# Kernel optimization log

Measured on AMD Instinct MI355X. Metric: run time of the kernel, lower is better.

The kernel has to match this reference:

```python
import jax, jax.numpy as jnp
import numpy as np

N = 25000      # nodes
E = 400000     # directed edges (avg degree 16)
FN = 32        # node feature dim
FE = 16        # edge feature dim
H = 16         # hidden_state_size
M = 16         # message_size
ITERS = 3      # mp_iterations


def setup_inputs() -> dict:
    key = jax.random.key(0)
    ks = jax.random.split(key, 16)
    s = 0.1
    return {
        "node_features": jax.random.normal(ks[0], (N, FN), jnp.float32),
        "edge_features": jax.random.normal(ks[1], (E, FE), jnp.float32),
        # Initial dense
        "W_init": jax.random.normal(ks[2], (FN, H), jnp.float32) * s,
        "b_init": jnp.zeros((H,), jnp.float32),
        # edge_net dense: FE -> M*H
        "W_edge": jax.random.normal(ks[3], (FE, M * H), jnp.float32) * s,
        "b_edge": jnp.zeros((M * H,), jnp.float32),
        # GRU (keras default, reset_after=True), input dim 1, units H, gate order z|r|h
        "Wi_gru": jax.random.normal(ks[4], (1, 3 * H), jnp.float32) * s,
        "Wh_gru": jax.random.normal(ks[5], (H, 3 * H), jnp.float32) * s,
        "bi_gru": jnp.zeros((3 * H,), jnp.float32),
        "bh_gru": jnp.zeros((3 * H,), jnp.float32),
        # Readout denses -> 1 output
        "W_ri": jax.random.normal(ks[6], (2 * H, 1), jnp.float32) * s,
        "b_ri": jnp.zeros((1,), jnp.float32),
        "W_rj": jax.random.normal(ks[7], (H, 1), jnp.float32) * s,
        "b_rj": jnp.zeros((1,), jnp.float32),
        # graph structure (directed edges): message to `receivers[e]` from `senders[e]`
        "receivers": jax.random.randint(ks[8], (E,), 0, N, jnp.int32),
        "senders": jax.random.randint(ks[9], (E,), 0, N, jnp.int32),
    }


def _gru_seq(seq, Wi, Wh, bi, bh):
    # seq: [N, T] sequence of scalars per node; keras GRU, reset_after=True, units=H
    n = seq.shape[0]
    xs = seq.T[:, :, None]  # [T, N, 1]
    h0 = jnp.zeros((n, H), seq.dtype)

    def step(h, x_t):
        gx = x_t @ Wi + bi            # [N, 3H]
        gh = h @ Wh + bh              # [N, 3H]
        xz, xr, xh = jnp.split(gx, 3, axis=1)
        hz, hr, hh = jnp.split(gh, 3, axis=1)
        z = jax.nn.sigmoid(xz + hz)
        r = jax.nn.sigmoid(xr + hr)
        hcand = jnp.tanh(xh + r * hh)
        h_new = z * h + (1.0 - z) * hcand
        return h_new, None

    h_final, _ = jax.lax.scan(step, h0, xs)
    return h_final


def reference(node_features, edge_features, W_init, b_init, W_edge, b_edge,
              Wi_gru, Wh_gru, bi_gru, bh_gru, W_ri, b_ri, W_rj, b_rj,
              receivers, senders):
    # Initial hidden state
    hidden0 = node_features @ W_init + b_init   # [N, H]
    hidden = hidden0

    # edge_net(edge) reshaped to per-edge matrices [E, M, H] (constant across iterations)
    edge_mats = (edge_features @ W_edge + b_edge).reshape(E, M, H)

    for _ in range(ITERS):
        h_nb = hidden[senders]                                  # [E, H]
        msg = jnp.einsum("emh,eh->em", edge_mats, h_nb)        # [E, M] matvec per edge
        messages = jax.ops.segment_sum(msg, receivers, num_segments=N)  # sum aggregation
        seq = jnp.concatenate([hidden, messages], axis=1)       # [N, H+M]
        hidden = _gru_seq(seq, Wi_gru, Wh_gru, bi_gru, bh_gru)  # [N, H]

    # Readout
    i = jnp.concatenate([hidden, hidden0], axis=1) @ W_ri + b_ri  # [N, 1]
    j = hidden @ W_rj + b_rj                                      # [N, 1]
    return jnp.sum(i * j, axis=0)                                 # [1]
```

## Files before the change

kernel.cpp:

```cpp
#include <hip/hip_runtime.h>

#define N_NODES 25000
#define N_EDGES 400000

__device__ __forceinline__ float fast_sigmoid(float x) {
    return __builtin_amdgcn_rcpf(1.0f + __expf(-x));
}
__device__ __forceinline__ float fast_tanh(float x) {
    return 1.0f - 2.0f * __builtin_amdgcn_rcpf(__expf(2.0f * x) + 1.0f);
}

#define SWZF(x, k) __int_as_float(__builtin_amdgcn_ds_swizzle(__float_as_int(x), ((k) << 10) | 0x1F))
#define BCAST16(x, t) __int_as_float(__builtin_amdgcn_ds_swizzle(__float_as_int(x), ((t) << 5) | 0x10))

__global__ void __launch_bounds__(256) k_init(
        const float* __restrict__ nf, const float* __restrict__ Wini,
        const float* __restrict__ bini,
        float* __restrict__ hidden0, float* __restrict__ hid,
        int* __restrict__ cnt, int* __restrict__ rcnt)
{
    int gtid = blockIdx.x * 256 + threadIdx.x;
    if (gtid <= N_NODES) { cnt[gtid] = 0; rcnt[gtid] = 0; }
    int node = gtid >> 4;
    int j = gtid & 15;
    if (node >= N_NODES) return;

    const float4* nf4 = (const float4*)(nf + node * 32);
    float acc = bini[j];
#pragma unroll
    for (int g = 0; g < 8; ++g) {
        float4 v = nf4[g];
        acc = fmaf(v.x, Wini[(g*4+0)*16 + j], acc);
        acc = fmaf(v.y, Wini[(g*4+1)*16 + j], acc);
        acc = fmaf(v.z, Wini[(g*4+2)*16 + j], acc);
        acc = fmaf(v.w, Wini[(g*4+3)*16 + j], acc);
    }
    hidden0[node*16 + j] = acc;
    hid[node*16 + j] = acc;
}

__global__ void __launch_bounds__(256) k_rank(const int* __restrict__ send,
        const int* __restrict__ recv,
        int* __restrict__ cnt, int* __restrict__ rcnt,
        int* __restrict__ rank_s, int* __restrict__ rank_r)
{
    int e = blockIdx.x * 256 + threadIdx.x;
    if (e < N_EDGES) {
        rank_s[e] = atomicAdd(&cnt[send[e]], 1);
        rank_r[e] = atomicAdd(&rcnt[recv[e]], 1);
    }
}

#define SCAN_TOT 25600
__global__ void __launch_bounds__(1024) k_scan2(
        const int* __restrict__ cnt,  int* __restrict__ row_ptr,
        const int* __restrict__ rcnt, int* __restrict__ rrow_ptr,
        float* __restrict__ out)
{
    __shared__ int data[SCAN_TOT];
    __shared__ int sums[1024];
    int t = threadIdx.x;
    const int CH = 25;

    const int* SRC = blockIdx.x ? rcnt : cnt;
    int* DST = blockIdx.x ? rrow_ptr : row_ptr;

    for (int i = t; i < SCAN_TOT; i += 1024)
        data[i] = (i < N_NODES) ? SRC[i] : 0;
    __syncthreads();

    int base = t * CH;
    int s = 0;
#pragma unroll
    for (int i = 0; i < CH; ++i) s += data[base + i];
    sums[t] = s;
    __syncthreads();

    for (int off = 1; off < 1024; off <<= 1) {
        int add = (t >= off) ? sums[t - off] : 0;
        __syncthreads();
        sums[t] += add;
        __syncthreads();
    }
    int run = sums[t] - s;

#pragma unroll
    for (int i = 0; i < CH; ++i) {
        int v = data[base + i];
        data[base + i] = run;
        run += v;
    }
    __syncthreads();

    for (int i = t; i < N_NODES; i += 1024)
        DST[i] = data[i];
    if (t == 0) {
        if (blockIdx.x == 0) { row_ptr[N_NODES] = N_EDGES; out[0] = 0.0f; }
        else                 { rrow_ptr[N_NODES] = N_EDGES; }
    }
}

__global__ void __launch_bounds__(256) k_place(const int* __restrict__ send,
        const int* __restrict__ recv,
        const int* __restrict__ rank_s, const int* __restrict__ rank_r,
        const int* __restrict__ row_ptr, const int* __restrict__ rrow_ptr,
        const float* __restrict__ ef, float* __restrict__ efp,
        int* __restrict__ rp)
{
    int e = blockIdx.x * 256 + threadIdx.x;
    if (e < N_EDGES) {
        int pos = row_ptr[send[e]] + rank_s[e];
        rp[pos] = rrow_ptr[recv[e]] + rank_r[e];
        const float4* src = (const float4*)(ef + (size_t)e * 16);
        float4* dst = (float4*)(efp + (size_t)pos * 16);
        float4 a = src[0], b = src[1], c = src[2], d = src[3];
        dst[0] = a; dst[1] = b; dst[2] = c; dst[3] = d;
    }
}

#define MCHUNK 512
#define MSG16(E0,E1,E2,E3) ( \
    ( fmaf((E0).w,q[3],  fmaf((E0).z,q[2],  fmaf((E0).y,q[1],  fmaf((E0).x,q[0],  qb)))) \
    + fmaf((E1).w,q[7],  fmaf((E1).z,q[6],  fmaf((E1).y,q[5],  fmaf((E1).x,q[4],  0.0f)))) ) \
  + ( fmaf((E2).w,q[11], fmaf((E2).z,q[10], fmaf((E2).y,q[9],  fmaf((E2).x,q[8],  0.0f)))) \
    + fmaf((E3).w,q[15], fmaf((E3).z,q[14], fmaf((E3).y,q[13], fmaf((E3).x,q[12], 0.0f)))) ) )

__global__ void __launch_bounds__(256) k_msg(
        const float* __restrict__ hid, const float* __restrict__ efp,
        const int* __restrict__ rp,
        const float* __restrict__ We, const float* __restrict__ be,
        const int* __restrict__ row_ptr,
        float* __restrict__ tmp)
{
    __shared__ float sef[MCHUNK * 16];
    __shared__ int   srp[MCHUNK];
    int tid = threadIdx.x;
    int grp = tid >> 4;
    int m   = tid & 15;
    int s   = blockIdx.x * 16 + grp;
    bool active = (s < N_NODES);
    int sc = active ? s : 0;

    int s0 = blockIdx.x * 16;
    int blk_beg = row_ptr[s0];
    int s1 = s0 + 16; if (s1 > N_NODES) s1 = N_NODES;
    int blk_end = row_ptr[s1];

    int beg = active ? row_ptr[s]     : 0;
    int end = active ? row_ptr[s + 1] : 0;

    float h[16];
    {
        const float4* h4 = (const float4*)(hid + sc*16);
        float4 a = h4[0], b = h4[1], c = h4[2], d = h4[3];
        h[0]=a.x; h[1]=a.y; h[2]=a.z;  h[3]=a.w;
        h[4]=b.x; h[5]=b.y; h[6]=b.z;  h[7]=b.w;
        h[8]=c.x; h[9]=c.y; h[10]=c.z; h[11]=c.w;
        h[12]=d.x; h[13]=d.y; h[14]=d.z; h[15]=d.w;
    }
    float q[16];
#pragma unroll
    for (int f = 0; f < 16; ++f) {
        const float4* wf = (const float4*)(We + f*256 + m*16);
        float4 a = wf[0], b = wf[1], c = wf[2], d = wf[3];
        float acc;
        acc  = a.x*h[0]  + a.y*h[1]  + a.z*h[2]  + a.w*h[3];
        acc += b.x*h[4]  + b.y*h[5]  + b.z*h[6]  + b.w*h[7];
        acc += c.x*h[8]  + c.y*h[9]  + c.z*h[10] + c.w*h[11];
        acc += d.x*h[12] + d.y*h[13] + d.z*h[14] + d.w*h[15];
        q[f] = acc;
    }
    float qb;
    {
        const float4* bf = (const float4*)(be + m*16);
        float4 a = bf[0], b = bf[1], c = bf[2], d = bf[3];
        qb  = a.x*h[0]  + a.y*h[1]  + a.z*h[2]  + a.w*h[3];
        qb += b.x*h[4]  + b.y*h[5]  + b.z*h[6]  + b.w*h[7];
        qb += c.x*h[8]  + c.y*h[9]  + c.z*h[10] + c.w*h[11];
        qb += d.x*h[12] + d.y*h[13] + d.z*h[14] + d.w*h[15];
    }

    for (int cbeg = blk_beg; cbeg < blk_end; cbeg += MCHUNK) {
        int cend = cbeg + MCHUNK; if (cend > blk_end) cend = blk_end;
        int nedge = cend - cbeg;
        int nfl = nedge * 4;
        __syncthreads();
        {
            const float4* gsrc = (const float4*)(efp + (size_t)cbeg * 16);
            float4* ldst = (float4*)sef;
            for (int i = tid; i < nfl; i += 256) ldst[i] = gsrc[i];
            for (int i = tid; i < nedge; i += 256) srp[i] = rp[cbeg + i];
        }
        __syncthreads();

        int lo = beg > cbeg ? beg : cbeg;
        int hi = end < cend ? end : cend;
        int i = lo;
        for (; i + 2 <= hi; i += 2) {
            const float4* l0 = (const float4*)(sef + (size_t)(i   - cbeg) * 16);
            const float4* l1 = (const float4*)(sef + (size_t)(i+1 - cbeg) * 16);
            float4 A0=l0[0], A1=l0[1], A2=l0[2], A3=l0[3];
            float4 B0=l1[0], B1=l1[1], B2=l1[2], B3=l1[3];
            int r0 = srp[i   - cbeg];
            int r1 = srp[i+1 - cbeg];
            float v0 = MSG16(A0, A1, A2, A3);
            float v1 = MSG16(B0, B1, B2, B3);
            tmp[(size_t)r0*16 + m] = v0;
            tmp[(size_t)r1*16 + m] = v1;
        }
        for (; i < hi; ++i) {
            const float4* l0 = (const float4*)(sef + (size_t)(i - cbeg) * 16);
            float4 A0=l0[0], A1=l0[1], A2=l0[2], A3=l0[3];
            int r0 = srp[i - cbeg];
            tmp[(size_t)r0*16 + m] = MSG16(A0, A1, A2, A3);
        }
    }
}

__global__ void __launch_bounds__(256) k_gru(
        const float* __restrict__ hid_in, const float* __restrict__ tmp,
        const int* __restrict__ rrow_ptr,
        const float* __restrict__ Wi, const float* __restrict__ Wh,
        const float* __restrict__ bi, const float* __restrict__ bh,
        float* __restrict__ hid_out)
{
    int gtid = blockIdx.x * 256 + threadIdx.x;
    int node = gtid >> 4;
    int j = gtid & 15;
    if (node >= N_NODES) return;

    float s0 = 0.0f, s1 = 0.0f, s2 = 0.0f, s3 = 0.0f;
    {
        int beg = rrow_ptr[node];
        int end = rrow_ptr[node + 1];
        const float* p = tmp + (size_t)beg * 16 + j;
        int d = end - beg;
        int i = 0;
        for (; i + 8 <= d; i += 8) {
            float a0 = p[(i+0)*16];
            float a1 = p[(i+1)*16];
            float a2 = p[(i+2)*16];
            float a3 = p[(i+3)*16];
            float a4 = p[(i+4)*16];
            float a5 = p[(i+5)*16];
            float a6 = p[(i+6)*16];
            float a7 = p[(i+7)*16];
            s0 += a0; s1 += a1; s2 += a2; s3 += a3;
            s0 += a4; s1 += a5; s2 += a6; s3 += a7;
        }
        for (; i < d; ++i) s0 += p[i*16];
    }
    float msg_own = (s0 + s1) + (s2 + s3);
    float h_own = hid_in[node*16 + j];

    float Wz[16], Wr[16], Wc[16];
#pragma unroll
    for (int k = 0; k < 16; ++k) {
        int l = j ^ k;
        Wz[k] = Wh[l*48 + j];
        Wr[k] = Wh[l*48 + 16 + j];
        Wc[k] = Wh[l*48 + 32 + j];
    }
    float Wiz = Wi[j], Wir = Wi[16+j], Wih = Wi[32+j];
    float cz   = bi[j] + bh[j];
    float cr   = bi[16+j] + bh[16+j];
    float bih_ = bi[32+j];
    float bhh_ = bh[32+j];

    float hn = 0.0f;

#define STEPK2(k0, k1) { \
        float va = SWZF(hn, k0); float vb = SWZF(hn, k1); \
        az0 = fmaf(va, Wz[k0], az0); az1 = fmaf(vb, Wz[k1], az1); \
        ar0 = fmaf(va, Wr[k0], ar0); ar1 = fmaf(vb, Wr[k1], ar1); \
        ac0 = fmaf(va, Wc[k0], ac0); ac1 = fmaf(vb, Wc[k1], ac1); }

#define GRUSTEP(XV) { \
        float xv = (XV); \
        float v1 = SWZF(hn, 1); \
        float az0 = fmaf(xv, Wiz, cz); \
        float ar0 = fmaf(xv, Wir, cr); \
        float ac0 = bhh_; \
        az0 = fmaf(hn, Wz[0], az0); \
        ar0 = fmaf(hn, Wr[0], ar0); \
        ac0 = fmaf(hn, Wc[0], ac0); \
        float az1 = v1 * Wz[1]; \
        float ar1 = v1 * Wr[1]; \
        float ac1 = v1 * Wc[1]; \
        STEPK2(2,3)   STEPK2(4,5)   STEPK2(6,7) \
        STEPK2(8,9)   STEPK2(10,11) STEPK2(12,13) \
        STEPK2(14,15) \
        float z  = fast_sigmoid(az0 + az1); \
        float r  = fast_sigmoid(ar0 + ar1); \
        float hc = fast_tanh(fmaf(xv, Wih, bih_) + r * (ac0 + ac1)); \
        hn = fmaf(z, hn - hc, hc); }

    GRUSTEP(BCAST16(h_own, 0))  GRUSTEP(BCAST16(h_own, 1))
    GRUSTEP(BCAST16(h_own, 2))  GRUSTEP(BCAST16(h_own, 3))
    GRUSTEP(BCAST16(h_own, 4))  GRUSTEP(BCAST16(h_own, 5))
    GRUSTEP(BCAST16(h_own, 6))  GRUSTEP(BCAST16(h_own, 7))
    GRUSTEP(BCAST16(h_own, 8))  GRUSTEP(BCAST16(h_own, 9))
    GRUSTEP(BCAST16(h_own, 10)) GRUSTEP(BCAST16(h_own, 11))
    GRUSTEP(BCAST16(h_own, 12)) GRUSTEP(BCAST16(h_own, 13))
    GRUSTEP(BCAST16(h_own, 14)) GRUSTEP(BCAST16(h_own, 15))
    GRUSTEP(BCAST16(msg_own, 0))  GRUSTEP(BCAST16(msg_own, 1))
    GRUSTEP(BCAST16(msg_own, 2))  GRUSTEP(BCAST16(msg_own, 3))
    GRUSTEP(BCAST16(msg_own, 4))  GRUSTEP(BCAST16(msg_own, 5))
    GRUSTEP(BCAST16(msg_own, 6))  GRUSTEP(BCAST16(msg_own, 7))
    GRUSTEP(BCAST16(msg_own, 8))  GRUSTEP(BCAST16(msg_own, 9))
    GRUSTEP(BCAST16(msg_own, 10)) GRUSTEP(BCAST16(msg_own, 11))
    GRUSTEP(BCAST16(msg_own, 12)) GRUSTEP(BCAST16(msg_own, 13))
    GRUSTEP(BCAST16(msg_own, 14)) GRUSTEP(BCAST16(msg_own, 15))
#undef GRUSTEP
#undef STEPK2

    hid_out[node*16 + j] = hn;
}

__global__ void __launch_bounds__(256) k_readout(
        const float* __restrict__ hid, const float* __restrict__ hid0,
        const float* __restrict__ Wri, const float* __restrict__ bri,
        const float* __restrict__ Wrj, const float* __restrict__ brj,
        float* __restrict__ out)
{
    int n = blockIdx.x * 256 + threadIdx.x;
    float val = 0.0f;
    if (n < N_NODES) {
        const float4* h4 = (const float4*)(hid + n * 16);
        const float4* g4 = (const float4*)(hid0 + n * 16);
        float iv = bri[0];
        float jv = brj[0];
#pragma unroll
        for (int g = 0; g < 4; ++g) {
            float4 h  = h4[g];
            float4 h0 = g4[g];
            iv = fmaf(h.x,  Wri[g*4+0], iv);  iv = fmaf(h.y,  Wri[g*4+1], iv);
            iv = fmaf(h.z,  Wri[g*4+2], iv);  iv = fmaf(h.w,  Wri[g*4+3], iv);
            iv = fmaf(h0.x, Wri[16+g*4+0], iv); iv = fmaf(h0.y, Wri[16+g*4+1], iv);
            iv = fmaf(h0.z, Wri[16+g*4+2], iv); iv = fmaf(h0.w, Wri[16+g*4+3], iv);
            jv = fmaf(h.x,  Wrj[g*4+0], jv);  jv = fmaf(h.y,  Wrj[g*4+1], jv);
            jv = fmaf(h.z,  Wrj[g*4+2], jv);  jv = fmaf(h.w,  Wrj[g*4+3], jv);
        }
        val = iv * jv;
    }
#pragma unroll
    for (int off = 32; off > 0; off >>= 1)
        val += __shfl_xor(val, off, 64);
    __shared__ float wsum[4];
    int w = threadIdx.x >> 6;
    if ((threadIdx.x & 63) == 0) wsum[w] = val;
    __syncthreads();
    if (threadIdx.x == 0)
        atomicAdd(out, wsum[0] + wsum[1] + wsum[2] + wsum[3]);
}

extern "C" void kernel_launch(void* const* d_in, const int* in_sizes, int n_in,
                              void* d_out, int out_size, void* d_ws, size_t ws_size,
                              hipStream_t stream)
{
    const float* node_features = (const float*)d_in[0];
    const float* edge_features = (const float*)d_in[1];
    const float* W_init = (const float*)d_in[2];
    const float* b_init = (const float*)d_in[3];
    const float* W_edge = (const float*)d_in[4];
    const float* b_edge = (const float*)d_in[5];
    const float* Wi_gru = (const float*)d_in[6];
    const float* Wh_gru = (const float*)d_in[7];
    const float* bi_gru = (const float*)d_in[8];
    const float* bh_gru = (const float*)d_in[9];
    const float* W_ri = (const float*)d_in[10];
    const float* b_ri = (const float*)d_in[11];
    const float* W_rj = (const float*)d_in[12];
    const float* b_rj = (const float*)d_in[13];
    const int* receivers = (const int*)d_in[14];
    const int* senders   = (const int*)d_in[15];
    float* out = (float*)d_out;

    float* fb      = (float*)d_ws;
    float* hidden0 = fb;
    float* hidA    = fb + 400000;
    float* hidB    = fb + 800000;
    float* tmp     = fb + 1200000;
    float* efp     = fb + 7600000;
    int* ib       = (int*)(fb + 14000000);
    int* cnt      = ib;
    int* row_ptr  = ib + 25024;
    int* rcnt     = ib + 50048;
    int* rrow_ptr = ib + 75072;
    int* rp       = ib + 100096;
    int* rank_s   = ib + 500096;
    int* rank_r   = ib + 900096;

    dim3 b256(256);
    int grid_n16 = (N_NODES * 16 + 255) / 256;
    int grid_e   = (N_EDGES + 255) / 256;
    int grid_n   = (N_NODES + 255) / 256;
    int grid_blk = (N_NODES + 15) / 16;

    k_init<<<grid_n16, b256, 0, stream>>>(node_features, W_init, b_init,
                                          hidden0, hidA, cnt, rcnt);
    k_rank<<<grid_e, b256, 0, stream>>>(senders, receivers, cnt, rcnt,
                                        rank_s, rank_r);
    k_scan2<<<2, 1024, 0, stream>>>(cnt, row_ptr, rcnt, rrow_ptr, out);
    k_place<<<grid_e, b256, 0, stream>>>(senders, receivers, rank_s, rank_r,
                                         row_ptr, rrow_ptr,
                                         edge_features, efp, rp);

    float* hin = hidA;
    float* hout = hidB;
    for (int it = 0; it < 3; ++it) {
        k_msg<<<grid_blk, b256, 0, stream>>>(hin, efp, rp,
                                             W_edge, b_edge, row_ptr, tmp);
        k_gru<<<grid_n16, b256, 0, stream>>>(hin, tmp, rrow_ptr,
                                             Wi_gru, Wh_gru, bi_gru, bh_gru, hout);
        float* t = hin; hin = hout; hout = t;
    }

    k_readout<<<grid_n, b256, 0, stream>>>(hin, hidden0, W_ri, b_ri, W_rj, b_rj, out);
}
```

Measured before the change: 402.5 us.

## Fuse GRU update with next iteration's message computation

Moves the GRU update and the following message pass into one kernel, k_fused. Each 16-lane group computes its node's new hidden state and keeps it in registers through swizzle broadcasts, then computes that node's outgoing messages straight away. This removes two kernel launches and a round trip of the hidden state through global memory. In exchange it double-buffers the message buffer to avoid read/write races, which grows the workspace, and halves the shared-memory edge chunk size to 256. Occupancy and register pressure may get worse, since the GRU and message phases now share one kernel.

```diff
diff --git a/kernel.cpp b/kernel.cpp
--- a/kernel.cpp
+++ b/kernel.cpp
@@ -13,151 +13,107 @@
 #define SWZF(x, k) __int_as_float(__builtin_amdgcn_ds_swizzle(__float_as_int(x), ((k) << 10) | 0x1F))
 #define BCAST16(x, t) __int_as_float(__builtin_amdgcn_ds_swizzle(__float_as_int(x), ((t) << 5) | 0x10))
 
-__global__ void __launch_bounds__(256) k_init(
-        const float* __restrict__ nf, const float* __restrict__ Wini,
-        const float* __restrict__ bini,
-        float* __restrict__ hidden0, float* __restrict__ hid,
-        int* __restrict__ cnt, int* __restrict__ rcnt)
-{
-    int gtid = blockIdx.x * 256 + threadIdx.x;
-    if (gtid <= N_NODES) { cnt[gtid] = 0; rcnt[gtid] = 0; }
-    int node = gtid >> 4;
-    int j = gtid & 15;
-    if (node >= N_NODES) return;
-
-    const float4* nf4 = (const float4*)(nf + node * 32);
-    float acc = bini[j];
-#pragma unroll
-    for (int g = 0; g < 8; ++g) {
-        float4 v = nf4[g];
-        acc = fmaf(v.x, Wini[(g*4+0)*16 + j], acc);
-        acc = fmaf(v.y, Wini[(g*4+1)*16 + j], acc);
-        acc = fmaf(v.z, Wini[(g*4+2)*16 + j], acc);
-        acc = fmaf(v.w, Wini[(g*4+3)*16 + j], acc);
-    }
-    hidden0[node*16 + j] = acc;
-    hid[node*16 + j] = acc;
-}
-
-__global__ void __launch_bounds__(256) k_rank(const int* __restrict__ send,
-        const int* __restrict__ recv,
-        int* __restrict__ cnt, int* __restrict__ rcnt,
-        int* __restrict__ rank_s, int* __restrict__ rank_r)
-{
-    int e = blockIdx.x * 256 + threadIdx.x;
-    if (e < N_EDGES) {
-        rank_s[e] = atomicAdd(&cnt[send[e]], 1);
-        rank_r[e] = atomicAdd(&rcnt[recv[e]], 1);
-    }
-}
-
-#define SCAN_TOT 25600
-__global__ void __launch_bounds__(1024) k_scan2(
-        const int* __restrict__ cnt,  int* __restrict__ row_ptr,
-        const int* __restrict__ rcnt, int* __restrict__ rrow_ptr,
-        float* __restrict__ out)
-{
-    __shared__ int data[SCAN_TOT];
-    __shared__ int sums[1024];
-    int t = threadIdx.x;
-    const int CH = 25;
-
-    const int* SRC = blockIdx.x ? rcnt : cnt;
-    int* DST = blockIdx.x ? rrow_ptr : row_ptr;
-
-    for (int i = t; i < SCAN_TOT; i += 1024)
-        data[i] = (i < N_NODES) ? SRC[i] : 0;
-    __syncthreads();
-
-    int base = t * CH;
-    int s = 0;
-#pragma unroll
-    for (int i = 0; i < CH; ++i) s += data[base + i];
-    sums[t] = s;
-    __syncthreads();
-
-    for (int off = 1; off < 1024; off <<= 1) {
-        int add = (t >= off) ? sums[t - off] : 0;
-        __syncthreads();
-        sums[t] += add;
-        __syncthreads();
-    }
-    int run = sums[t] - s;
-
-#pragma unroll
-    for (int i = 0; i < CH; ++i) {
-        int v = data[base + i];
-        data[base + i] = run;
-        run += v;
-    }
-    __syncthreads();
-
-    for (int i = t; i < N_NODES; i += 1024)
-        DST[i] = data[i];
-    if (t == 0) {
-        if (blockIdx.x == 0) { row_ptr[N_NODES] = N_EDGES; out[0] = 0.0f; }
-        else                 { rrow_ptr[N_NODES] = N_EDGES; }
-    }
-}
-
-__global__ void __launch_bounds__(256) k_place(const int* __restrict__ send,
-        const int* __restrict__ recv,
-        const int* __restrict__ rank_s, const int* __restrict__ rank_r,
-        const int* __restrict__ row_ptr, const int* __restrict__ rrow_ptr,
-        const float* __restrict__ ef, float* __restrict__ efp,
-        int* __restrict__ rp)
-{
-    int e = blockIdx.x * 256 + threadIdx.x;
-    if (e < N_EDGES) {
-        int pos = row_ptr[send[e]] + rank_s[e];
-        rp[pos] = rrow_ptr[recv[e]] + rank_r[e];
-        const float4* src = (const float4*)(ef + (size_t)e * 16);
-        float4* dst = (float4*)(efp + (size_t)pos * 16);
-        float4 a = src[0], b = src[1], c = src[2], d = src[3];
-        dst[0] = a; dst[1] = b; dst[2] = c; dst[3] = d;
-    }
-}
-
-#define MCHUNK 512
+#define STEPK2(k0, k1) { \
+        float va = SWZF(hn, k0); float vb = SWZF(hn, k1); \
+        az0 = fmaf(va, Wz[k0], az0); az1 = fmaf(vb, Wz[k1], az1); \
+        ar0 = fmaf(va, Wr[k0], ar0); ar1 = fmaf(vb, Wr[k1], ar1); \
+        ac0 = fmaf(va, Wc[k0], ac0); ac1 = fmaf(vb, Wc[k1], ac1); }
+
+#define GRUSTEP(XV) { \
+        float xv = (XV); \
+        float v1 = SWZF(hn, 1); \
+        float az0 = fmaf(xv, Wiz, cz); \
+        float ar0 = fmaf(xv, Wir, cr); \
+        float ac0 = bhh_; \
+        az0 = fmaf(hn, Wz[0], az0); \
+        ar0 = fmaf(hn, Wr[0], ar0); \
+        ac0 = fmaf(hn, Wc[0], ac0); \
+        float az1 = v1 * Wz[1]; \
+        float ar1 = v1 * Wr[1]; \
+        float ac1 = v1 * Wc[1]; \
+        STEPK2(2,3)   STEPK2(4,5)   STEPK2(6,7) \
+        STEPK2(8,9)   STEPK2(10,11) STEPK2(12,13) \
+        STEPK2(14,15) \
+        float z  = fast_sigmoid(az0 + az1); \
+        float r  = fast_sigmoid(ar0 + ar1); \
+        float hc = fast_tanh(fmaf(xv, Wih, bih_) + r * (ac0 + ac1)); \
+        hn = fmaf(z, hn - hc, hc); }
+
+__device__ __forceinline__ float gru32(float h_own, float msg_own, int j,
+        const float* __restrict__ Wi, const float* __restrict__ Wh,
+        const float* __restrict__ bi, const float* __restrict__ bh)
+{
+    float Wz[16], Wr[16], Wc[16];
+#pragma unroll
+    for (int k = 0; k < 16; ++k) {
+        int l = j ^ k;
+        Wz[k] = Wh[l*48 + j];
+        Wr[k] = Wh[l*48 + 16 + j];
+        Wc[k] = Wh[l*48 + 32 + j];
+    }
+    float Wiz = Wi[j], Wir = Wi[16+j], Wih = Wi[32+j];
+    float cz   = bi[j] + bh[j];
+    float cr   = bi[16+j] + bh[16+j];
+    float bih_ = bi[32+j];
+    float bhh_ = bh[32+j];
+
+    float hn = 0.0f;
+    GRUSTEP(BCAST16(h_own, 0))  GRUSTEP(BCAST16(h_own, 1))
+    GRUSTEP(BCAST16(h_own, 2))  GRUSTEP(BCAST16(h_own, 3))
+    GRUSTEP(BCAST16(h_own, 4))  GRUSTEP(BCAST16(h_own, 5))
+    GRUSTEP(BCAST16(h_own, 6))  GRUSTEP(BCAST16(h_own, 7))
+    GRUSTEP(BCAST16(h_own, 8))  GRUSTEP(BCAST16(h_own, 9))
+    GRUSTEP(BCAST16(h_own, 10)) GRUSTEP(BCAST16(h_own, 11))
+    GRUSTEP(BCAST16(h_own, 12)) GRUSTEP(BCAST16(h_own, 13))
+    GRUSTEP(BCAST16(h_own, 14)) GRUSTEP(BCAST16(h_own, 15))
+    GRUSTEP(BCAST16(msg_own, 0))  GRUSTEP(BCAST16(msg_own, 1))
+    GRUSTEP(BCAST16(msg_own, 2))  GRUSTEP(BCAST16(msg_own, 3))
+    GRUSTEP(BCAST16(msg_own, 4))  GRUSTEP(BCAST16(msg_own, 5))
+    GRUSTEP(BCAST16(msg_own, 6))  GRUSTEP(BCAST16(msg_own, 7))
+    GRUSTEP(BCAST16(msg_own, 8))  GRUSTEP(BCAST16(msg_own, 9))
+    GRUSTEP(BCAST16(msg_own, 10)) GRUSTEP(BCAST16(msg_own, 11))
+    GRUSTEP(BCAST16(msg_own, 12)) GRUSTEP(BCAST16(msg_own, 13))
+    GRUSTEP(BCAST16(msg_own, 14)) GRUSTEP(BCAST16(msg_own, 15))
+    return hn;
+}
+
+__device__ __forceinline__ float gather16(const float* __restrict__ tmp,
+        int beg, int end, int j)
+{
+    const float* p = tmp + (size_t)beg * 16 + j;
+    int d = end - beg;
+    float s0 = 0.0f, s1 = 0.0f, s2 = 0.0f, s3 = 0.0f;
+    int i = 0;
+    for (; i + 8 <= d; i += 8) {
+        float a0 = p[(i+0)*16];
+        float a1 = p[(i+1)*16];
+        float a2 = p[(i+2)*16];
+        float a3 = p[(i+3)*16];
+        float a4 = p[(i+4)*16];
+        float a5 = p[(i+5)*16];
+        float a6 = p[(i+6)*16];
+        float a7 = p[(i+7)*16];
+        s0 += a0; s1 += a1; s2 += a2; s3 += a3;
+        s0 += a4; s1 += a5; s2 += a6; s3 += a7;
+    }
+    for (; i < d; ++i) s0 += p[i*16];
+    return (s0 + s1) + (s2 + s3);
+}
+
+#define MCHUNK 256
 #define MSG16(E0,E1,E2,E3) ( \
     ( fmaf((E0).w,q[3],  fmaf((E0).z,q[2],  fmaf((E0).y,q[1],  fmaf((E0).x,q[0],  qb)))) \
     + fmaf((E1).w,q[7],  fmaf((E1).z,q[6],  fmaf((E1).y,q[5],  fmaf((E1).x,q[4],  0.0f)))) ) \
   + ( fmaf((E2).w,q[11], fmaf((E2).z,q[10], fmaf((E2).y,q[9],  fmaf((E2).x,q[8],  0.0f)))) \
     + fmaf((E3).w,q[15], fmaf((E3).z,q[14], fmaf((E3).y,q[13], fmaf((E3).x,q[12], 0.0f)))) ) )
 
-__global__ void __launch_bounds__(256) k_msg(
-        const float* __restrict__ hid, const float* __restrict__ efp,
-        const int* __restrict__ rp,
+__device__ __forceinline__ void msg_phase(const float* __restrict__ h, int m,
+        int tid, int blk_first, int beg, int end,
+        const float* __restrict__ efp, const int* __restrict__ rp,
         const float* __restrict__ We, const float* __restrict__ be,
-        const int* __restrict__ row_ptr,
-        float* __restrict__ tmp)
-{
-    __shared__ float sef[MCHUNK * 16];
-    __shared__ int   srp[MCHUNK];
-    int tid = threadIdx.x;
-    int grp = tid >> 4;
-    int m   = tid & 15;
-    int s   = blockIdx.x * 16 + grp;
-    bool active = (s < N_NODES);
-    int sc = active ? s : 0;
-
-    int s0 = blockIdx.x * 16;
-    int blk_beg = row_ptr[s0];
-    int s1 = s0 + 16; if (s1 > N_NODES) s1 = N_NODES;
-    int blk_end = row_ptr[s1];
-
-    int beg = active ? row_ptr[s]     : 0;
-    int end = active ? row_ptr[s + 1] : 0;
-
-    float h[16];
-    {
-        const float4* h4 = (const float4*)(hid + sc*16);
-        float4 a = h4[0], b = h4[1], c = h4[2], d = h4[3];
-        h[0]=a.x; h[1]=a.y; h[2]=a.z;  h[3]=a.w;
-        h[4]=b.x; h[5]=b.y; h[6]=b.z;  h[7]=b.w;
-        h[8]=c.x; h[9]=c.y; h[10]=c.z; h[11]=c.w;
-        h[12]=d.x; h[13]=d.y; h[14]=d.z; h[15]=d.w;
-    }
+        const int* __restrict__ row_ptr, float* __restrict__ tmp,
+        float* __restrict__ sef, int* __restrict__ srp)
+{
     float q[16];
 #pragma unroll
     for (int f = 0; f < 16; ++f) {
@@ -179,6 +135,10 @@
         qb += c.x*h[8]  + c.y*h[9]  + c.z*h[10] + c.w*h[11];
         qb += d.x*h[12] + d.y*h[13] + d.z*h[14] + d.w*h[15];
     }
+
+    int blk_beg = row_ptr[blk_first];
+    int s1 = blk_first + 16; if (s1 > N_NODES) s1 = N_NODES;
+    int blk_end = row_ptr[s1];
 
     for (int cbeg = blk_beg; cbeg < blk_end; cbeg += MCHUNK) {
         int cend = cbeg + MCHUNK; if (cend > blk_end) cend = blk_end;
@@ -217,6 +177,143 @@
     }
 }
 
+__global__ void __launch_bounds__(256) k_init(
+        const float* __restrict__ nf, const float* __restrict__ Wini,
+        const float* __restrict__ bini,
+        float* __restrict__ hidden0, float* __restrict__ hid,
+        int* __restrict__ cnt, int* __restrict__ rcnt)
+{
+    int gtid = blockIdx.x * 256 + threadIdx.x;
+    if (gtid <= N_NODES) { cnt[gtid] = 0; rcnt[gtid] = 0; }
+    int node = gtid >> 4;
+    int j = gtid & 15;
+    if (node >= N_NODES) return;
+
+    const float4* nf4 = (const float4*)(nf + node * 32);
+    float acc = bini[j];
+#pragma unroll
+    for (int g = 0; g < 8; ++g) {
+        float4 v = nf4[g];
+        acc = fmaf(v.x, Wini[(g*4+0)*16 + j], acc);
+        acc = fmaf(v.y, Wini[(g*4+1)*16 + j], acc);
+        acc = fmaf(v.z, Wini[(g*4+2)*16 + j], acc);
+        acc = fmaf(v.w, Wini[(g*4+3)*16 + j], acc);
+    }
+    hidden0[node*16 + j] = acc;
+    hid[node*16 + j] = acc;
+}
+
+__global__ void __launch_bounds__(256) k_rank(const int* __restrict__ send,
+        const int* __restrict__ recv,
+        int* __restrict__ cnt, int* __restrict__ rcnt,
+        int* __restrict__ rank_s, int* __restrict__ rank_r)
+{
+    int e = blockIdx.x * 256 + threadIdx.x;
+    if (e < N_EDGES) {
+        rank_s[e] = atomicAdd(&cnt[send[e]], 1);
+        rank_r[e] = atomicAdd(&rcnt[recv[e]], 1);
+    }
+}
+
+#define SCAN_TOT 25600
+__global__ void __launch_bounds__(1024) k_scan2(
+        const int* __restrict__ cnt,  int* __restrict__ row_ptr,
+        const int* __restrict__ rcnt, int* __restrict__ rrow_ptr,
+        float* __restrict__ out)
+{
+    __shared__ int data[SCAN_TOT];
+    __shared__ int sums[1024];
+    int t = threadIdx.x;
+    const int CH = 25;
+
+    const int* SRC = blockIdx.x ? rcnt : cnt;
+    int* DST = blockIdx.x ? rrow_ptr : row_ptr;
+
+    for (int i = t; i < SCAN_TOT; i += 1024)
+        data[i] = (i < N_NODES) ? SRC[i] : 0;
+    __syncthreads();
+
+    int base = t * CH;
+    int s = 0;
+#pragma unroll
+    for (int i = 0; i < CH; ++i) s += data[base + i];
+    sums[t] = s;
+    __syncthreads();
+
+    for (int off = 1; off < 1024; off <<= 1) {
+        int add = (t >= off) ? sums[t - off] : 0;
+        __syncthreads();
+        sums[t] += add;
+        __syncthreads();
+    }
+    int run = sums[t] - s;
+
+#pragma unroll
+    for (int i = 0; i < CH; ++i) {
+        int v = data[base + i];
+        data[base + i] = run;
+        run += v;
+    }
+    __syncthreads();
+
+    for (int i = t; i < N_NODES; i += 1024)
+        DST[i] = data[i];
+    if (t == 0) {
+        if (blockIdx.x == 0) { row_ptr[N_NODES] = N_EDGES; out[0] = 0.0f; }
+        else                 { rrow_ptr[N_NODES] = N_EDGES; }
+    }
+}
+
+__global__ void __launch_bounds__(256) k_place(const int* __restrict__ send,
+        const int* __restrict__ recv,
+        const int* __restrict__ rank_s, const int* __restrict__ rank_r,
+        const int* __restrict__ row_ptr, const int* __restrict__ rrow_ptr,
+        const float* __restrict__ ef, float* __restrict__ efp,
+        int* __restrict__ rp)
+{
+    int e = blockIdx.x * 256 + threadIdx.x;
+    if (e < N_EDGES) {
+        int pos = row_ptr[send[e]] + rank_s[e];
+        rp[pos] = rrow_ptr[recv[e]] + rank_r[e];
+        const float4* src = (const float4*)(ef + (size_t)e * 16);
+        float4* dst = (float4*)(efp + (size_t)pos * 16);
+        float4 a = src[0], b = src[1], c = src[2], d = src[3];
+        dst[0] = a; dst[1] = b; dst[2] = c; dst[3] = d;
+    }
+}
+
+__global__ void __launch_bounds__(256) k_msg(
+        const float* __restrict__ hid, const float* __restrict__ efp,
+        const int* __restrict__ rp,
+        const float* __restrict__ We, const float* __restrict__ be,
+        const int* __restrict__ row_ptr,
+        float* __restrict__ tmp)
+{
+    __shared__ float sef[MCHUNK * 16];
+    __shared__ int   srp[MCHUNK];
+    int tid = threadIdx.x;
+    int grp = tid >> 4;
+    int m   = tid & 15;
+    int s   = blockIdx.x * 16 + grp;
+    bool active = (s < N_NODES);
+    int sc = active ? s : 0;
+
+    int beg = active ? row_ptr[s]     : 0;
+    int end = active ? row_ptr[s + 1] : 0;
+
+    float h[16];
+    {
+        const float4* h4 = (const float4*)(hid + sc*16);
+        float4 a = h4[0], b = h4[1], c = h4[2], d = h4[3];
+        h[0]=a.x; h[1]=a.y; h[2]=a.z;  h[3]=a.w;
+        h[4]=b.x; h[5]=b.y; h[6]=b.z;  h[7]=b.w;
+        h[8]=c.x; h[9]=c.y; h[10]=c.z; h[11]=c.w;
+        h[12]=d.x; h[13]=d.y; h[14]=d.z; h[15]=d.w;
+    }
+    msg_phase(h, m, tid, blockIdx.x * 16, beg, end,
+              efp, rp, We, be, row_ptr, tmp, sef, srp);
+}
+
 __global__ void __launch_bounds__(256) k_gru(
         const float* __restrict__ hid_in, const float* __restrict__ tmp,
         const int* __restrict__ rrow_ptr,
@@ -229,92 +326,52 @@
     int j = gtid & 15;
     if (node >= N_NODES) return;
 
-    float s0 = 0.0f, s1 = 0.0f, s2 = 0.0f, s3 = 0.0f;
-    {
-        int beg = rrow_ptr[node];
-        int end = rrow_ptr[node + 1];
-        const float* p = tmp + (size_t)beg * 16 + j;
-        int d = end - beg;
-        int i = 0;
-        for (; i + 8 <= d; i += 8) {
-            float a0 = p[(i+0)*16];
-            float a1 = p[(i+1)*16];
-            float a2 = p[(i+2)*16];
-            float a3 = p[(i+3)*16];
-            float a4 = p[(i+4)*16];
-            float a5 = p[(i+5)*16];
-            float a6 = p[(i+6)*16];
-            float a7 = p[(i+7)*16];
-            s0 += a0; s1 += a1; s2 += a2; s3 += a3;
-            s0 += a4; s1 += a5; s2 += a6; s3 += a7;
-        }
-        for (; i < d; ++i) s0 += p[i*16];
-    }
-    float msg_own = (s0 + s1) + (s2 + s3);
+    float msg_own = gather16(tmp, rrow_ptr[node], rrow_ptr[node + 1], j);
     float h_own = hid_in[node*16 + j];
-
-    float Wz[16], Wr[16], Wc[16];
-#pragma unroll
-    for (int k = 0; k < 16; ++k) {
-        int l = j ^ k;
-        Wz[k] = Wh[l*48 + j];
-        Wr[k] = Wh[l*48 + 16 + j];
-        Wc[k] = Wh[l*48 + 32 + j];
-    }
-    float Wiz = Wi[j], Wir = Wi[16+j], Wih = Wi[32+j];
-    float cz   = bi[j] + bh[j];
-    float cr   = bi[16+j] + bh[16+j];
-    float bih_ = bi[32+j];
-    float bhh_ = bh[32+j];
-
-    float hn = 0.0f;
-
-#define STEPK2(k0, k1) { \
-        float va = SWZF(hn, k0); float vb = SWZF(hn, k1); \
-        az0 = fmaf(va, Wz[k0], az0); az1 = fmaf(vb, Wz[k1], az1); \
-        ar0 = fmaf(va, Wr[k0], ar0); ar1 = fmaf(vb, Wr[k1], ar1); \
-        ac0 = fmaf(va, Wc[k0], ac0); ac1 = fmaf(vb, Wc[k1], ac1); }
-
-#define GRUSTEP(XV) { \
-        float xv = (XV); \
-        float v1 = SWZF(hn, 1); \
-        float az0 = fmaf(xv, Wiz, cz); \
-        float ar0 = fmaf(xv, Wir, cr); \
-        float ac0 = bhh_; \
-        az0 = fmaf(hn, Wz[0], az0); \
-        ar0 = fmaf(hn, Wr[0], ar0); \
-        ac0 = fmaf(hn, Wc[0], ac0); \
-        float az1 = v1 * Wz[1]; \
-        float ar1 = v1 * Wr[1]; \
-        float ac1 = v1 * Wc[1]; \
-        STEPK2(2,3)   STEPK2(4,5)   STEPK2(6,7) \
-        STEPK2(8,9)   STEPK2(10,11) STEPK2(12,13) \
-        STEPK2(14,15) \
-        float z  = fast_sigmoid(az0 + az1); \
-        float r  = fast_sigmoid(ar0 + ar1); \
-        float hc = fast_tanh(fmaf(xv, Wih, bih_) + r * (ac0 + ac1)); \
-        hn = fmaf(z, hn - hc, hc); }
-
-    GRUSTEP(BCAST16(h_own, 0))  GRUSTEP(BCAST16(h_own, 1))
-    GRUSTEP(BCAST16(h_own, 2))  GRUSTEP(BCAST16(h_own, 3))
-    GRUSTEP(BCAST16(h_own, 4))  GRUSTEP(BCAST16(h_own, 5))
-    GRUSTEP(BCAST16(h_own, 6))  GRUSTEP(BCAST16(h_own, 7))
-    GRUSTEP(BCAST16(h_own, 8))  GRUSTEP(BCAST16(h_own, 9))
-    GRUSTEP(BCAST16(h_own, 10)) GRUSTEP(BCAST16(h_own, 11))
-    GRUSTEP(BCAST16(h_own, 12)) GRUSTEP(BCAST16(h_own, 13))
-    GRUSTEP(BCAST16(h_own, 14)) GRUSTEP(BCAST16(h_own, 15))
-    GRUSTEP(BCAST16(msg_own, 0))  GRUSTEP(BCAST16(msg_own, 1))
-    GRUSTEP(BCAST16(msg_own, 2))  GRUSTEP(BCAST16(msg_own, 3))
-    GRUSTEP(BCAST16(msg_own, 4))  GRUSTEP(BCAST16(msg_own, 5))
-    GRUSTEP(BCAST16(msg_own, 6))  GRUSTEP(BCAST16(msg_own, 7))
-    GRUSTEP(BCAST16(msg_own, 8))  GRUSTEP(BCAST16(msg_own, 9))
-    GRUSTEP(BCAST16(msg_own, 10)) GRUSTEP(BCAST16(msg_own, 11))
-    GRUSTEP(BCAST16(msg_own, 12)) GRUSTEP(BCAST16(msg_own, 13))
-    GRUSTEP(BCAST16(msg_own, 14)) GRUSTEP(BCAST16(msg_own, 15))
-#undef GRUSTEP
-#undef STEPK2
-
+    float hn = gru32(h_own, msg_own, j, Wi, Wh, bi, bh);
     hid_out[node*16 + j] = hn;
+}
+
+__global__ void __launch_bounds__(256) k_fused(
+        const float* __restrict__ hid_in, const float* __restrict__ tmp_in,
+        const int* __restrict__ rrow_ptr,
+        const float* __restrict__ Wi, const float* __restrict__ Wh,
+        const float* __restrict__ bi, const float* __restrict__ bh,
+        float* __restrict__ hid_out,
+        const float* __restrict__ efp, const int* __restrict__ rp,
+        const float* __restrict__ We, const float* __restrict__ be,
+        const int* __restrict__ row_ptr, float* __restrict__ tmp_out)
+{
+    __shared__ float sef[MCHUNK * 16];
+    __shared__ int   srp[MCHUNK];
+    int tid = threadIdx.x;
+    int grp = tid >> 4;
+    int j   = tid & 15;
+    int node = blockIdx.x * 16 + grp;
+    bool active = (node < N_NODES);
+    int nc = active ? node : 0;
+
+    int gbeg = rrow_ptr[nc];
+    int gend = active ? rrow_ptr[nc + 1] : gbeg;
+    float msg_own = gather16(tmp_in, gbeg, gend, j);
+    float h_own = hid_in[nc*16 + j];
+    float hn = gru32(h_own, msg_own, j, Wi, Wh, bi, bh);
+    if (active) hid_out[node*16 + j] = hn;
+
+    float h[16];
+    h[0]  = BCAST16(hn, 0);   h[1]  = BCAST16(hn, 1);
+    h[2]  = BCAST16(hn, 2);   h[3]  = BCAST16(hn, 3);
+    h[4]  = BCAST16(hn, 4);   h[5]  = BCAST16(hn, 5);
+    h[6]  = BCAST16(hn, 6);   h[7]  = BCAST16(hn, 7);
+    h[8]  = BCAST16(hn, 8);   h[9]  = BCAST16(hn, 9);
+    h[10] = BCAST16(hn, 10);  h[11] = BCAST16(hn, 11);
+    h[12] = BCAST16(hn, 12);  h[13] = BCAST16(hn, 13);
+    h[14] = BCAST16(hn, 14);  h[15] = BCAST16(hn, 15);
+
+    int beg = active ? row_ptr[node]     : 0;
+    int end = active ? row_ptr[node + 1] : 0;
+    msg_phase(h, j, tid, blockIdx.x * 16, beg, end,
+              efp, rp, We, be, row_ptr, tmp_out, sef, srp);
 }
 
 __global__ void __launch_bounds__(256) k_readout(
@@ -380,9 +437,10 @@
     float* hidden0 = fb;
     float* hidA    = fb + 400000;
     float* hidB    = fb + 800000;
-    float* tmp     = fb + 1200000;
-    float* efp     = fb + 7600000;
-    int* ib       = (int*)(fb + 14000000);
+    float* tmpA    = fb + 1200000;
+    float* tmpB    = fb + 7600000;
+    float* efp     = fb + 14000000;
+    int* ib       = (int*)(fb + 20400000);
     int* cnt      = ib;
     int* row_ptr  = ib + 25024;
     int* rcnt     = ib + 50048;
@@ -406,15 +464,20 @@
                                          row_ptr, rrow_ptr,
                                          edge_features, efp, rp);
 
-    float* hin = hidA;
-    float* hout = hidB;
-    for (int it = 0; it < 3; ++it) {
-        k_msg<<<grid_blk, b256, 0, stream>>>(hin, efp, rp,
-                                             W_edge, b_edge, row_ptr, tmp);
-        k_gru<<<grid_n16, b256, 0, stream>>>(hin, tmp, rrow_ptr,
-                                             Wi_gru, Wh_gru, bi_gru, bh_gru, hout);
-        float* t = hin; hin = hout; hout = t;
-    }
-
-    k_readout<<<grid_n, b256, 0, stream>>>(hin, hidden0, W_ri, b_ri, W_rj, b_rj, out);
-}
+    k_msg<<<grid_blk, b256, 0, stream>>>(hidA, efp, rp,
+                                         W_edge, b_edge, row_ptr, tmpA);
+    k_fused<<<grid_blk, b256, 0, stream>>>(hidA, tmpA, rrow_ptr,
+                                           Wi_gru, Wh_gru, bi_gru, bh_gru,
+                                           hidB,
+                                           efp, rp, W_edge, b_edge, row_ptr,
+                                           tmpB);
+    k_fused<<<grid_blk, b256, 0, stream>>>(hidB, tmpB, rrow_ptr,
+                                           Wi_gru, Wh_gru, bi_gru, bh_gru,
+                                           hidA,
+                                           efp, rp, W_edge, b_edge, row_ptr,
+                                           tmpA);
+    k_gru<<<grid_n16, b256, 0, stream>>>(hidA, tmpA, rrow_ptr,
+                                         Wi_gru, Wh_gru, bi_gru, bh_gru, hidB);
+
+    k_readout<<<grid_n, b256, 0, stream>>>(hidB, hidden0, W_ri, b_ri, W_rj, b_rj, out);
+}
```

Result: faster. 379.1 us (-5.8%).
